# Optimization experiments

Measured on AMD Instinct MI355X. Metric: run time of the kernel, lower is better.

The kernel has to match this reference:

```python
import jax, jax.numpy as jnp
import numpy as np

NUM_LEVELS = 16
COARSEST = 16
FINEST = 1024
TABLE_SIZE = 524288  # max_hash_table_entries per level
FEAT = 2             # hash_table_feature_dim
DENSITY_W = 64
COLOR_W = 64
N_POINTS = 262144

PRIMES = jnp.array([1, 2654435761, 805459861], dtype=jnp.uint32)
# 8 cube corners: 1 -> ceil coordinate, 0 -> floor coordinate (matches source vertex_0..vertex_7)
CORNER_SEL = np.array([[1,1,1],[1,1,0],[1,0,1],[0,1,1],[1,0,0],[0,1,0],[0,0,1],[0,0,0]], dtype=bool)


def hash_encode(position, hash_table):
    # position: (N,3) in [0,1); hash_table: (NUM_LEVELS*TABLE_SIZE, FEAT)
    levels = jnp.arange(NUM_LEVELS)
    growth = jnp.exp((jnp.log(float(FINEST)) - jnp.log(float(COARSEST))) / (NUM_LEVELS - 1))
    scalings = jnp.floor(COARSEST * growth ** levels)            # (L,)
    scaled = position[:, None, :] * scalings[None, :, None]       # (N,L,3)
    floor = jnp.floor(scaled)
    ceil = jnp.ceil(scaled)
    sel = jnp.asarray(CORNER_SEL)[None, None]                     # (1,1,8,3)
    corners = jnp.where(sel, ceil[:, :, None, :], floor[:, :, None, :]).astype(jnp.uint32)  # (N,L,8,3)
    h = corners * PRIMES                                          # uint32 wrap-around mul
    idx = jnp.bitwise_xor(jnp.bitwise_xor(h[..., 0], h[..., 1]), h[..., 2]) % TABLE_SIZE
    idx = idx + (levels[None, :, None] * TABLE_SIZE).astype(jnp.uint32)  # (N,L,8)
    feats = hash_table[idx]                                       # (N,L,8,F) gather
    frac = scaled - floor                                         # (N,L,3)
    w = jnp.prod(jnp.where(sel, frac[:, :, None, :], 1.0 - frac[:, :, None, :]), axis=-1)  # (N,L,8)
    out = jnp.sum(feats * w[..., None], axis=2)                   # trilinear interp -> (N,L,F)
    return out.reshape(out.shape[0], NUM_LEVELS * FEAT)           # (N,32)


def sh_encode(d):
    # fourth-order spherical harmonics, vectorized over (N,3)
    x, y, z = d[:, 0], d[:, 1], d[:, 2]
    xx, yy, zz = x * x, y * y, z * z
    comps = [
        0.28209479177387814 * jnp.ones_like(x),
        0.4886025119029199 * y,
        0.4886025119029199 * z,
        0.4886025119029199 * x,
        1.0925484305920792 * x * y,
        1.0925484305920792 * y * z,
        0.9461746957575601 * zz - 0.31539156525252,
        1.0925484305920792 * x * z,
        0.5462742152960396 * (xx - yy),
        0.5900435899266435 * y * (3 * xx - yy),
        2.890611442640554 * x * y * z,
        0.4570457994644658 * y * (5 * zz - 1),
        0.3731763325901154 * z * (5 * zz - 3),
        0.4570457994644658 * x * (5 * zz - 1),
        1.445305721320277 * z * (xx - yy),
        0.5900435899266435 * x * (xx - 3 * yy),
    ]
    return jnp.stack(comps, axis=-1)  # (N,16)


def setup_inputs() -> dict:
    key = jax.random.key(0)
    ks = jax.random.split(key, 16)
    N = N_POINTS
    position = jax.random.uniform(ks[0], (N, 3), dtype=jnp.float32)
    direction = jax.random.normal(ks[1], (N, 3), dtype=jnp.float32)
    hash_table = jax.random.normal(ks[2], (NUM_LEVELS * TABLE_SIZE, FEAT), dtype=jnp.float32) * 1e-2
    enc_dim = NUM_LEVELS * FEAT  # 32
    def dense(k, fi, fo):
        return jax.random.normal(k, (fi, fo), dtype=jnp.float32) * (1.0 / np.sqrt(fi))
    return {
        "position": position,
        "direction": direction,
        "hash_table": hash_table,
        "w_d1": dense(ks[3], enc_dim, DENSITY_W), "b_d1": jnp.zeros((DENSITY_W,), jnp.float32),
        "w_d2": dense(ks[4], DENSITY_W, 16),      "b_d2": jnp.zeros((16,), jnp.float32),
        "w_c1": dense(ks[5], 16 + 16, COLOR_W),   "b_c1": jnp.zeros((COLOR_W,), jnp.float32),
        "w_c2": dense(ks[6], COLOR_W, COLOR_W),   "b_c2": jnp.zeros((COLOR_W,), jnp.float32),
        "w_c3": dense(ks[7], COLOR_W, 3),         "b_c3": jnp.zeros((3,), jnp.float32),
    }


def reference(position, direction, hash_table, w_d1, b_d1, w_d2, b_d2,
              w_c1, b_c1, w_c2, b_c2, w_c3, b_c3):
    enc_pos = hash_encode(position, hash_table)               # (N,32)
    h = jax.nn.relu(enc_pos @ w_d1 + b_d1)                    # (N,64)
    density = h @ w_d2 + b_d2                                 # (N,16)
    enc_dir = sh_encode(direction)                            # (N,16)
    x = jnp.concatenate([density, enc_dir], axis=-1)          # (N,32)
    x = jax.nn.relu(x @ w_c1 + b_c1)
    x = jax.nn.relu(x @ w_c2 + b_c2)
    x = x @ w_c3 + b_c3                                       # (N,3)
    color = jax.nn.sigmoid(x)                                 # high_dynamic_range=False
    return (density, color)
```

## Files before the change

### kernel.cpp

```cpp
#include <hip/hip_runtime.h>
#include <stdint.h>

#define NPTS 262144
#define TBL 524288u
#define TBL_MASK 524287u
#define NBINS 32768

#define WS_TAB_OFF   0u
#define WS_TAB_BYTES (11u * 524288u * 4u)
#define WS_ENC_OFF   WS_TAB_BYTES
#define WS_ENC_BYTES (16u * (uint32_t)NPTS * 4u)
#define WS_W_OFF     (WS_ENC_OFF + WS_ENC_BYTES)
#define WS_W_U32     4736
#define WS_HIST_OFF  (WS_W_OFF + WS_W_U32 * 4u)
#define WS_KEY_OFF   (WS_HIST_OFF + NBINS * 4u)
#define WS_IDX_OFF   (WS_KEY_OFF + (uint32_t)NPTS * 4u)
#define WS_PS_OFF    (WS_IDX_OFF + (uint32_t)NPTS * 4u)
#define WS_DS_OFF    (WS_PS_OFF + (uint32_t)NPTS * 12u)
#define WS_NEED_SORT ((size_t)WS_DS_OFF + (size_t)NPTS * 12u)
#define WS_NEED      ((size_t)WS_HIST_OFF)

#define PW_D1 0
#define PW_D2 1024
#define PW_C1 1536
#define PW_C2 2560
#define PW_C3 4608

typedef __attribute__((ext_vector_type(8))) _Float16 half8;
typedef __attribute__((ext_vector_type(4))) float f32x4;

__device__ const float d_scale[16] = {16.f, 21.f, 27.f, 36.f, 48.f, 64.f, 84.f, 111.f,
                                      147.f, 194.f, 256.f, 337.f, 445.f, 588.f, 776.f, 1024.f};

__device__ const uint16_t SEG_START[8][4] = {
    {0, 512, 683, 1024},
    {0, 512, 683, 854},
    {0, 512, 682, 1024},
    {0, 512, 768, 1024},
    {0, 512, 768, 1024},
    {0, 512, 768, 1024},
    {0, 512, 768, 1024},
    {0, 512, 1024, 1024},
};
__device__ const int8_t SEG_LEV[8][4] = {
    {9, 7, 2, 0}, {10, 7, 2, 1}, {11, 7, 1, 0}, {12, 6, 0, 0},
    {13, 6, 0, 0}, {14, 4, 3, 0}, {15, 4, 3, 0}, {8, 5, 0, 0},
};
__device__ const uint16_t SEG_CB[8][4] = {
    {0, 0, 0, 0}, {0, 171, 341, 0}, {0, 342, 170, 0}, {0, 0, 0, 0},
    {0, 256, 256, 0}, {0, 0, 0, 0}, {0, 256, 256, 0}, {0, 0, 0, 0},
};

__device__ __forceinline__ uint16_t f2h(float f) {
    _Float16 h = (_Float16)f;
    return __builtin_bit_cast(uint16_t, h);
}
__device__ __forceinline__ uint32_t pack2(float lo, float hi) {
    return (uint32_t)f2h(lo) | ((uint32_t)f2h(hi) << 16);
}
__device__ __forceinline__ float h2f_lo(uint32_t v) {
    return (float)__builtin_bit_cast(_Float16, (uint16_t)(v & 0xffffu));
}
__device__ __forceinline__ float h2f_hi(uint32_t v) {
    return (float)__builtin_bit_cast(_Float16, (uint16_t)(v >> 16));
}

__device__ __forceinline__ half8 bfrag_p(const uint32_t* __restrict__ Wp, int N, int kofs, int nofs, int l) {
    const int kp0 = (kofs + ((l >> 4) << 3)) >> 1;
    const uint32_t* p = Wp + (size_t)kp0 * N + (nofs + (l & 15));
    union { uint32_t u[4]; half8 s; } r;
    r.u[0] = p[0 * N];
    r.u[1] = p[1 * N];
    r.u[2] = p[2 * N];
    r.u[3] = p[3 * N];
    return r.s;
}
__device__ __forceinline__ half8 bfrag3_p(const uint32_t* __restrict__ Wp, int kofs, int l) {
    const int kp0 = (kofs + ((l >> 4) << 3)) >> 1;
    const int n = l & 15;
    union { uint32_t u[4]; half8 s; } r;
    if (n < 3) {
        const uint32_t* p = Wp + (size_t)kp0 * 4 + n;
        r.u[0] = p[0]; r.u[1] = p[4]; r.u[2] = p[8]; r.u[3] = p[12];
    } else {
        r.u[0] = 0; r.u[1] = 0; r.u[2] = 0; r.u[3] = 0;
    }
    return r.s;
}

__device__ __forceinline__ half8 ld_a_h(const unsigned char* hcb, int mt, int kb, int l) {
    const int row = mt * 16 + (l & 15);
    uint32_t byte = (uint32_t)row * 128 + (uint32_t)kb * 64 + (uint32_t)((l >> 4) << 4);
    byte ^= (uint32_t)(row & 7) << 4;
    return *(const half8*)(hcb + byte);
}
__device__ __forceinline__ void st_h(unsigned char* hcb, int row, int col, float v) {
    uint32_t byte = (uint32_t)row * 128 + (uint32_t)col * 2;
    byte ^= (uint32_t)(row & 7) << 4;
    *(uint16_t*)(hcb + byte) = f2h(fmaxf(v, 0.f));
}

#define MFMA(a, b, c) __builtin_amdgcn_mfma_f32_16x16x32_f16((a), (b), (c), 0, 0, 0)

__device__ __forceinline__ uint32_t spread3(uint32_t x) {
    x &= 0x3FFu;
    x = (x | (x << 16)) & 0x030000FFu;
    x = (x | (x << 8))  & 0x0300F00Fu;
    x = (x | (x << 4))  & 0x030C30C3u;
    x = (x | (x << 2))  & 0x09249249u;
    return x;
}

__global__ void __launch_bounds__(256) khist(
    const float* __restrict__ g_pos, uint32_t* __restrict__ key, uint32_t* __restrict__ hist)
{
    const int p = blockIdx.x * 256 + threadIdx.x;
    const float px = g_pos[3 * p + 0];
    const float py = g_pos[3 * p + 1];
    const float pz = g_pos[3 * p + 2];
    const uint32_t cx = min(31u, (uint32_t)(px * 32.f));
    const uint32_t cy = min(31u, (uint32_t)(py * 32.f));
    const uint32_t cz = min(31u, (uint32_t)(pz * 32.f));
    const uint32_t k = spread3(cx) | (spread3(cy) << 1) | (spread3(cz) << 2);
    key[p] = k;
    atomicAdd(&hist[k], 1u);
}

__global__ void __launch_bounds__(1024) kscan(uint32_t* __restrict__ hist) {
    const int tid = threadIdx.x;
    const int lane = tid & 63, wid = tid >> 6;
    uint4* hp = (uint4*)(hist + tid * 32);
    uint4 a[8];
    #pragma unroll
    for (int i = 0; i < 8; ++i) a[i] = hp[i];
    uint32_t S = 0;
    #pragma unroll
    for (int i = 0; i < 8; ++i) S += a[i].x + a[i].y + a[i].z + a[i].w;

    uint32_t s = S;
    #pragma unroll
    for (int d = 1; d < 64; d <<= 1) {
        const uint32_t t = __shfl_up(s, d);
        if (lane >= d) s += t;
    }
    __shared__ uint32_t ws[16];
    if (lane == 63) ws[wid] = s;
    __syncthreads();
    uint32_t woff = 0;
    for (int w = 0; w < wid; ++w) woff += ws[w];
    uint32_t run = woff + (s - S);

    #pragma unroll
    for (int i = 0; i < 8; ++i) {
        uint4 v = a[i];
        uint4 o;
        o.x = run; run += v.x;
        o.y = run; run += v.y;
        o.z = run; run += v.z;
        o.w = run; run += v.w;
        hp[i] = o;
    }
}

__global__ void __launch_bounds__(256) convert_scatter(
    const float4* __restrict__ t5,
    uint4* __restrict__ o,
    const float* __restrict__ wd1, const float* __restrict__ wd2,
    const float* __restrict__ wc1, const float* __restrict__ wc2,
    const float* __restrict__ wc3, uint32_t* __restrict__ wp,
    const float* __restrict__ g_pos, const float* __restrict__ g_dir,
    const uint32_t* __restrict__ key,
    uint32_t* __restrict__ hist, uint32_t* __restrict__ out_idx,
    float* __restrict__ pos_sorted, float* __restrict__ dir_sorted,
    const int scatter_blocks)
{
    const int blk = blockIdx.x;
    if (blk < scatter_blocks) {
        const int p = blk * 256 + threadIdx.x;
        const uint32_t slot = atomicAdd(&hist[key[p]], 1u);
        out_idx[slot] = (uint32_t)p;
        pos_sorted[3 * slot + 0] = g_pos[3 * p + 0];
        pos_sorted[3 * slot + 1] = g_pos[3 * p + 1];
        pos_sorted[3 * slot + 2] = g_pos[3 * p + 2];
        dir_sorted[3 * slot + 0] = g_dir[3 * p + 0];
        dir_sorted[3 * slot + 1] = g_dir[3 * p + 1];
        dir_sorted[3 * slot + 2] = g_dir[3 * p + 2];
    } else {
        const int cb = blk - scatter_blocks;
        const int i = cb * 256 + threadIdx.x;
        const float4 a = t5[2 * i];
        const float4 b = t5[2 * i + 1];
        o[i] = make_uint4(pack2(a.x, a.y), pack2(a.z, a.w),
                          pack2(b.x, b.y), pack2(b.z, b.w));
        if (cb == 0) {
            const int tid = threadIdx.x;
            for (int j = tid; j < 1024; j += 256) {
                const int kp = j >> 6, n = j & 63;
                wp[PW_D1 + j] = pack2(wd1[(2 * kp) * 64 + n], wd1[(2 * kp + 1) * 64 + n]);
            }
            for (int j = tid; j < 512; j += 256) {
                const int kp = j >> 4, n = j & 15;
                wp[PW_D2 + j] = pack2(wd2[(2 * kp) * 16 + n], wd2[(2 * kp + 1) * 16 + n]);
            }
            for (int j = tid; j < 1024; j += 256) {
                const int kp = j >> 6, n = j & 63;
                wp[PW_C1 + j] = pack2(wc1[(2 * kp) * 64 + n], wc1[(2 * kp + 1) * 64 + n]);
            }
            for (int j = tid; j < 2048; j += 256) {
                const int kp = j >> 6, n = j & 63;
                wp[PW_C2 + j] = pack2(wc2[(2 * kp) * 64 + n], wc2[(2 * kp + 1) * 64 + n]);
            }
            for (int j = tid; j < 128; j += 256) {
                const int kp = j >> 2, n = j & 3;
                wp[PW_C3 + j] = (n < 3) ? pack2(wc3[(2 * kp) * 3 + n], wc3[(2 * kp + 1) * 3 + n]) : 0u;
            }
        }
    }
}

__global__ void __launch_bounds__(256) gather_enc2(
    const float* __restrict__ pos,
    const float* __restrict__ g_tab32,
    const uint32_t* __restrict__ tab16,
    uint32_t* __restrict__ enc)
{
    const int b = blockIdx.x;
    const int x8 = b & 7;
    const int sslot = b >> 3;
    int seg = 0;
    #pragma unroll
    for (int i = 1; i < 4; ++i) seg = (sslot >= (int)SEG_START[x8][i]) ? i : seg;
    const int lev = SEG_LEV[x8][seg];
    const int chunk = (int)SEG_CB[x8][seg] + (sslot - (int)SEG_START[x8][seg]);
    const int pbase = (chunk << 9) + threadIdx.x;

    const float s = d_scale[lev];

    float tx[2], ty[2], tz[2];
    uint32_t idx0[2][4], idx1[2][4];
    bool odd[2];
    #pragma unroll
    for (int q = 0; q < 2; ++q) {
        const int p = pbase + q * 256;
        const float px = pos[3 * p + 0];
        const float py = pos[3 * p + 1];
        const float pz = pos[3 * p + 2];
        const float sx = px * s, sy = py * s, sz = pz * s;
        const float fx = floorf(sx), fy = floorf(sy), fz = floorf(sz);
        tx[q] = sx - fx; ty[q] = sy - fy; tz[q] = sz - fz;
        const uint32_t x0 = (uint32_t)fx, x1 = (uint32_t)ceilf(sx);
        const uint32_t hy0 = (uint32_t)fy * 2654435761u, hy1 = (uint32_t)ceilf(sy) * 2654435761u;
        const uint32_t hz0 = (uint32_t)fz * 805459861u,  hz1 = (uint32_t)ceilf(sz) * 805459861u;
        odd[q] = (x0 & 1u) != 0u;
        #pragma unroll
        for (int cp = 0; cp < 4; ++cp) {
            const uint32_t hyz = ((cp & 1) ? hy1 : hy0) ^ ((cp & 2) ? hz1 : hz0);
            idx0[q][cp] = (x0 ^ hyz) & TBL_MASK;
            idx1[q][cp] = (x1 ^ hyz) & TBL_MASK;
        }
    }

    float e[2][2] = {{0.f, 0.f}, {0.f, 0.f}};
    if (lev >= 5) {
        const uint32_t* t = tab16 + (size_t)(lev - 5) * TBL;
        uint2 v2[2][4];
        #pragma unroll
        for (int q = 0; q < 2; ++q)
            #pragma unroll
            for (int cp = 0; cp < 4; ++cp)
                v2[q][cp] = *reinterpret_cast<const uint2*>(t + (idx0[q][cp] & ~1u));
        uint32_t fup[2][4];
        #pragma unroll
        for (int q = 0; q < 2; ++q)
            #pragma unroll
            for (int cp = 0; cp < 4; ++cp)
                fup[q][cp] = odd[q] ? t[idx1[q][cp]] : 0u;
        #pragma unroll
        for (int q = 0; q < 2; ++q) {
            #pragma unroll
            for (int cp = 0; cp < 4; ++cp) {
                const bool lo = (idx0[q][cp] & 1u) == 0u;
                const uint32_t v0 = lo ? v2[q][cp].x : v2[q][cp].y;
                uint32_t v1 = lo ? v2[q][cp].y : v2[q][cp].x;
                if (odd[q]) v1 = fup[q][cp];
                const float wyz = ((cp & 1) ? ty[q] : 1.f - ty[q]) * ((cp & 2) ? tz[q] : 1.f - tz[q]);
                const float w0 = (1.f - tx[q]) * wyz;
                const float w1 = tx[q] * wyz;
                e[q][0] = fmaf(h2f_lo(v0), w0, fmaf(h2f_lo(v1), w1, e[q][0]));
                e[q][1] = fmaf(h2f_hi(v0), w0, fmaf(h2f_hi(v1), w1, e[q][1]));
            }
        }
    } else {
        const float2* t = (const float2*)g_tab32 + (size_t)lev * TBL;
        float4 v2[2][4];
        #pragma unroll
        for (int q = 0; q < 2; ++q)
            #pragma unroll
            for (int cp = 0; cp < 4; ++cp)
                v2[q][cp] = *reinterpret_cast<const float4*>(t + (idx0[q][cp] & ~1u));
        float2 fup[2][4];
        #pragma unroll
        for (int q = 0; q < 2; ++q)
            #pragma unroll
            for (int cp = 0; cp < 4; ++cp)
                fup[q][cp] = odd[q] ? t[idx1[q][cp]] : make_float2(0.f, 0.f);
        #pragma unroll
        for (int q = 0; q < 2; ++q) {
            #pragma unroll
            for (int cp = 0; cp < 4; ++cp) {
                const bool lo = (idx0[q][cp] & 1u) == 0u;
                const float v0x = lo ? v2[q][cp].x : v2[q][cp].z;
                const float v0y = lo ? v2[q][cp].y : v2[q][cp].w;
                float v1x = lo ? v2[q][cp].z : v2[q][cp].x;
                float v1y = lo ? v2[q][cp].w : v2[q][cp].y;
                if (odd[q]) { v1x = fup[q][cp].x; v1y = fup[q][cp].y; }
                const float wyz = ((cp & 1) ? ty[q] : 1.f - ty[q]) * ((cp & 2) ? tz[q] : 1.f - tz[q]);
                const float w0 = (1.f - tx[q]) * wyz;
                const float w1 = tx[q] * wyz;
                e[q][0] = fmaf(v0x, w0, fmaf(v1x, w1, e[q][0]));
                e[q][1] = fmaf(v0y, w0, fmaf(v1y, w1, e[q][1]));
            }
        }
    }
    #pragma unroll
    for (int q = 0; q < 2; ++q)
        enc[(size_t)lev * NPTS + pbase + q * 256] = pack2(e[q][0], e[q][1]);
}

__global__ void __launch_bounds__(256, 3) nerf_mlp(
    const float* __restrict__ g_dir,
    const uint32_t* __restrict__ enc,
    const uint32_t* __restrict__ wp,
    const uint32_t* __restrict__ out_idx,
    const int use_perm,
    const float* __restrict__ g_bd1,
    const float* __restrict__ g_bd2,
    const float* __restrict__ g_bc1,
    const float* __restrict__ g_bc2,
    const float* __restrict__ g_bc3,
    float* __restrict__ g_out)
{
    __shared__ __align__(16) unsigned char s_lds[4 * 12288];
    unsigned char* wbase = s_lds + (threadIdx.x >> 6) * 12288;
    unsigned char* hcb  = wbase;
    unsigned char* xinb = wbase + 8192;

    const int l = threadIdx.x & 63;
    const int m_my = l >> 4;
    const int r_my = l & 15;
    const int wpt  = blockIdx.x * 256 + (threadIdx.x & 192);
    const int p    = wpt + l;

    #pragma unroll
    for (int kb = 0; kb < 4; ++kb) {
        uint4 w4;
        w4.x = enc[(size_t)(4 * kb + 0) * NPTS + p];
        w4.y = enc[(size_t)(4 * kb + 1) * NPTS + p];
        w4.z = enc[(size_t)(4 * kb + 2) * NPTS + p];
        w4.w = enc[(size_t)(4 * kb + 3) * NPTS + p];
        *(uint4*)(hcb + m_my * 1024 + (kb * 16 + r_my) * 16) = w4;
    }

    const float dx = g_dir[3 * p + 0];
    const float dy = g_dir[3 * p + 1];
    const float dz = g_dir[3 * p + 2];

    {
        const float xx = dx * dx, yy = dy * dy, zz = dz * dz;
        float s[16];
        s[0]  = 0.28209479177387814f;
        s[1]  = 0.4886025119029199f * dy;
        s[2]  = 0.4886025119029199f * dz;
        s[3]  = 0.4886025119029199f * dx;
        s[4]  = 1.0925484305920792f * dx * dy;
        s[5]  = 1.0925484305920792f * dy * dz;
        s[6]  = 0.9461746957575601f * zz - 0.31539156525252f;
        s[7]  = 1.0925484305920792f * dx * dz;
        s[8]  = 0.5462742152960396f * (xx - yy);
        s[9]  = 0.5900435899266435f * dy * (3.f * xx - yy);
        s[10] = 2.890611442640554f * dx * dy * dz;
        s[11] = 0.4570457994644658f * dy * (5.f * zz - 1.f);
        s[12] = 0.3731763325901154f * dz * (5.f * zz - 3.f);
        s[13] = 0.4570457994644658f * dx * (5.f * zz - 1.f);
        s[14] = 1.445305721320277f * dz * (xx - yy);
        s[15] = 0.5900435899266435f * dx * (xx - 3.f * yy);
        *(uint4*)(xinb + m_my * 1024 + (32 + r_my) * 16) =
            make_uint4(pack2(s[0], s[1]), pack2(s[2], s[3]), pack2(s[4], s[5]), pack2(s[6], s[7]));
        *(uint4*)(xinb + m_my * 1024 + (48 + r_my) * 16) =
            make_uint4(pack2(s[8], s[9]), pack2(s[10], s[11]), pack2(s[12], s[13]), pack2(s[14], s[15]));
    }

    const int cl = l & 15;
    const int rg = (l >> 4) << 2;

    {
        f32x4 acc[4][4];
        half8 B[4];
        #pragma unroll
        for (int nt = 0; nt < 4; ++nt) {
            B[nt] = bfrag_p(wp + PW_D1, 64, 0, nt * 16, l);
            const float b = g_bd1[nt * 16 + cl];
            #pragma unroll
            for (int mt = 0; mt < 4; ++mt) acc[mt][nt] = (f32x4){b, b, b, b};
        }
        #pragma unroll
        for (int mt = 0; mt < 4; ++mt) {
            const half8 A = *(const half8*)(hcb + mt * 1024 + l * 16);
            #pragma unroll
            for (int nt = 0; nt < 4; ++nt) acc[mt][nt] = MFMA(A, B[nt], acc[mt][nt]);
        }
        #pragma unroll
        for (int mt = 0; mt < 4; ++mt)
            #pragma unroll
            for (int nt = 0; nt < 4; ++nt)
                #pragma unroll
                for (int r = 0; r < 4; ++r)
                    st_h(hcb, mt * 16 + rg + r, nt * 16 + cl, acc[mt][nt][r]);
    }

    {
        const half8 B0 = bfrag_p(wp + PW_D2, 16, 0,  0, l);
        const half8 B1 = bfrag_p(wp + PW_D2, 16, 32, 0, l);
        const float b = g_bd2[cl];
        #pragma unroll
        for (int mt = 0; mt < 4; ++mt) {
            f32x4 acc = (f32x4){b, b, b, b};
            acc = MFMA(ld_a_h(hcb, mt, 0, l), B0, acc);
            acc = MFMA(ld_a_h(hcb, mt, 1, l), B1, acc);
            #pragma unroll
            for (int r = 0; r < 4; ++r) {
                const int pt = wpt + mt * 16 + rg + r;
                const uint32_t opt = use_perm ? out_idx[pt] : (uint32_t)pt;
                g_out[(size_t)opt * 16 + cl] = acc[r];
                const uint32_t byte = (uint32_t)mt * 1024
                                    + (uint32_t)(((cl >> 3) * 16 + rg + r) * 16) + (uint32_t)(cl & 7) * 2;
                *(uint16_t*)(xinb + byte) = f2h(acc[r]);
            }
        }
    }

    {
        f32x4 acc[4][4];
        half8 B[4];
        #pragma unroll
        for (int nt = 0; nt < 4; ++nt) {
            B[nt] = bfrag_p(wp + PW_C1, 64, 0, nt * 16, l);
            const float b = g_bc1[nt * 16 + cl];
            #pragma unroll
            for (int mt = 0; mt < 4; ++mt) acc[mt][nt] = (f32x4){b, b, b, b};
        }
        #pragma unroll
        for (int mt = 0; mt < 4; ++mt) {
            const half8 A = *(const half8*)(xinb + mt * 1024 + l * 16);
            #pragma unroll
            for (int nt = 0; nt < 4; ++nt) acc[mt][nt] = MFMA(A, B[nt], acc[mt][nt]);
        }
        #pragma unroll
        for (int mt = 0; mt < 4; ++mt)
            #pragma unroll
            for (int nt = 0; nt < 4; ++nt)
                #pragma unroll
                for (int r = 0; r < 4; ++r)
                    st_h(hcb, mt * 16 + rg + r, nt * 16 + cl, acc[mt][nt][r]);
    }

    {
        f32x4 acc[4][4];
        #pragma unroll
        for (int nt = 0; nt < 4; ++nt) {
            const float b = g_bc2[nt * 16 + cl];
            #pragma unroll
            for (int mt = 0; mt < 4; ++mt) acc[mt][nt] = (f32x4){b, b, b, b};
        }
        #pragma unroll
        for (int kb = 0; kb < 2; ++kb) {
            half8 A[4];
            #pragma unroll
            for (int mt = 0; mt < 4; ++mt) A[mt] = ld_a_h(hcb, mt, kb, l);
            #pragma unroll
            for (int nt = 0; nt < 4; ++nt) {
                const half8 B = bfrag_p(wp + PW_C2, 64, kb * 32, nt * 16, l);
                #pragma unroll
                for (int mt = 0; mt < 4; ++mt) acc[mt][nt] = MFMA(A[mt], B, acc[mt][nt]);
            }
        }
        #pragma unroll
        for (int mt = 0; mt < 4; ++mt)
            #pragma unroll
            for (int nt = 0; nt < 4; ++nt)
                #pragma unroll
                for (int r = 0; r < 4; ++r)
                    st_h(hcb, mt * 16 + rg + r, nt * 16 + cl, acc[mt][nt][r]);
    }

    {
        const half8 B0 = bfrag3_p(wp + PW_C3, 0, l);
        const half8 B1 = bfrag3_p(wp + PW_C3, 32, l);
        const float b = (cl < 3) ? g_bc3[cl] : 0.f;
        #pragma unroll
        for (int mt = 0; mt < 4; ++mt) {
            f32x4 acc = (f32x4){b, b, b, b};
            acc = MFMA(ld_a_h(hcb, mt, 0, l), B0, acc);
            acc = MFMA(ld_a_h(hcb, mt, 1, l), B1, acc);
            if (cl < 3) {
                #pragma unroll
                for (int r = 0; r < 4; ++r) {
                    const int pt = wpt + mt * 16 + rg + r;
                    const uint32_t opt = use_perm ? out_idx[pt] : (uint32_t)pt;
                    g_out[(size_t)NPTS * 16 + (size_t)opt * 3 + cl] = 1.f / (1.f + expf(-acc[r]));
                }
            }
        }
    }
}

extern "C" void kernel_launch(void* const* d_in, const int* in_sizes, int n_in,
                              void* d_out, int out_size, void* d_ws, size_t ws_size,
                              hipStream_t stream) {
    uint32_t* tab16 = (uint32_t*)((char*)d_ws + WS_TAB_OFF);
    uint32_t* enc   = (uint32_t*)((char*)d_ws + WS_ENC_OFF);
    uint32_t* wpk   = (uint32_t*)((char*)d_ws + WS_W_OFF);
    uint32_t* hist  = (uint32_t*)((char*)d_ws + WS_HIST_OFF);
    uint32_t* key   = (uint32_t*)((char*)d_ws + WS_KEY_OFF);
    uint32_t* oidx  = (uint32_t*)((char*)d_ws + WS_IDX_OFF);
    float*    psort = (float*)((char*)d_ws + WS_PS_OFF);
    float*    dsort = (float*)((char*)d_ws + WS_DS_OFF);

    const float* g_pos = (const float*)d_in[0];
    const float* g_dir = (const float*)d_in[1];
    const float* g_tab = (const float*)d_in[2];
    const float4* t5 = (const float4*)(g_tab + (size_t)2 * 5 * TBL);

    if (ws_size >= WS_NEED_SORT) {
        hipMemsetAsync(hist, 0, NBINS * 4, stream);
        khist<<<NPTS / 256, 256, 0, stream>>>(g_pos, key, hist);
        kscan<<<1, 1024, 0, stream>>>(hist);
        convert_scatter<<<1024 + 5632, 256, 0, stream>>>(
            t5, (uint4*)tab16,
            (const float*)d_in[3], (const float*)d_in[5],
            (const float*)d_in[7], (const float*)d_in[9],
            (const float*)d_in[11], wpk,
            g_pos, g_dir, key, hist, oidx, psort, dsort, 1024);
        gather_enc2<<<8192, 256, 0, stream>>>(psort, g_tab, tab16, enc);
        nerf_mlp<<<NPTS / 256, 256, 0, stream>>>(
            dsort, enc, wpk, oidx, 1,
            (const float*)d_in[4], (const float*)d_in[6],
            (const float*)d_in[8], (const float*)d_in[10],
            (const float*)d_in[12],
            (float*)d_out);
    } else {
        convert_scatter<<<5632, 256, 0, stream>>>(
            t5, (uint4*)tab16,
            (const float*)d_in[3], (const float*)d_in[5],
            (const float*)d_in[7], (const float*)d_in[9],
            (const float*)d_in[11], wpk,
            g_pos, g_dir, nullptr, nullptr, nullptr, nullptr, nullptr, 0);
        gather_enc2<<<8192, 256, 0, stream>>>(g_pos, g_tab, tab16, enc);
        nerf_mlp<<<NPTS / 256, 256, 0, stream>>>(
            g_dir, enc, wpk, nullptr, 0,
            (const float*)d_in[4], (const float*)d_in[6],
            (const float*)d_in[8], (const float*)d_in[10],
            (const float*)d_in[12],
            (float*)d_out);
    }
}
```

Baseline: 164.2 us.

## Split gather and MLP into chunks and overlap second gather with first MLP

```diff
diff --git a/kernel.cpp b/kernel.cpp
--- a/kernel.cpp
+++ b/kernel.cpp
@@ -5,6 +5,12 @@
 #define TBL 524288u
 #define TBL_MASK 524287u
 #define NBINS 32768
+
+#define CH_A 320
+#define CH_B 192
+#define GB_BLOCKS (16 * CH_B)
+#define MA_BLOCKS (CH_A * 2)
+#define MB_BLOCKS (CH_B * 2)
 
 #define WS_TAB_OFF   0u
 #define WS_TAB_BYTES (11u * 524288u * 4u)
@@ -31,25 +37,6 @@
 
 __device__ const float d_scale[16] = {16.f, 21.f, 27.f, 36.f, 48.f, 64.f, 84.f, 111.f,
                                       147.f, 194.f, 256.f, 337.f, 445.f, 588.f, 776.f, 1024.f};
-
-__device__ const uint16_t SEG_START[8][4] = {
-    {0, 512, 683, 1024},
-    {0, 512, 683, 854},
-    {0, 512, 682, 1024},
-    {0, 512, 768, 1024},
-    {0, 512, 768, 1024},
-    {0, 512, 768, 1024},
-    {0, 512, 768, 1024},
-    {0, 512, 1024, 1024},
-};
-__device__ const int8_t SEG_LEV[8][4] = {
-    {9, 7, 2, 0}, {10, 7, 2, 1}, {11, 7, 1, 0}, {12, 6, 0, 0},
-    {13, 6, 0, 0}, {14, 4, 3, 0}, {15, 4, 3, 0}, {8, 5, 0, 0},
-};
-__device__ const uint16_t SEG_CB[8][4] = {
-    {0, 0, 0, 0}, {0, 171, 341, 0}, {0, 342, 170, 0}, {0, 0, 0, 0},
-    {0, 256, 256, 0}, {0, 0, 0, 0}, {0, 256, 256, 0}, {0, 0, 0, 0},
-};
 
 __device__ __forceinline__ uint16_t f2h(float f) {
     _Float16 h = (_Float16)f;
@@ -218,20 +205,16 @@
     }
 }
 
-__global__ void __launch_bounds__(256) gather_enc2(
+__device__ __forceinline__ void gather_body(
+    const int b, const int chunk_lo,
     const float* __restrict__ pos,
     const float* __restrict__ g_tab32,
     const uint32_t* __restrict__ tab16,
     uint32_t* __restrict__ enc)
 {
-    const int b = blockIdx.x;
     const int x8 = b & 7;
-    const int sslot = b >> 3;
-    int seg = 0;
-    #pragma unroll
-    for (int i = 1; i < 4; ++i) seg = (sslot >= (int)SEG_START[x8][i]) ? i : seg;
-    const int lev = SEG_LEV[x8][seg];
-    const int chunk = (int)SEG_CB[x8][seg] + (sslot - (int)SEG_START[x8][seg]);
+    const int lev = ((b >> 3) & 1) ? (15 - x8) : x8;
+    const int chunk = chunk_lo + (b >> 4);
     const int pbase = (chunk << 9) + threadIdx.x;
 
     const float s = d_scale[lev];
@@ -327,7 +310,18 @@
         enc[(size_t)lev * NPTS + pbase + q * 256] = pack2(e[q][0], e[q][1]);
 }
 
-__global__ void __launch_bounds__(256, 3) nerf_mlp(
+__global__ void __launch_bounds__(256) gather_range(
+    const float* __restrict__ pos,
+    const float* __restrict__ g_tab32,
+    const uint32_t* __restrict__ tab16,
+    uint32_t* __restrict__ enc,
+    const int chunk_lo)
+{
+    gather_body(blockIdx.x, chunk_lo, pos, g_tab32, tab16, enc);
+}
+
+__device__ __forceinline__ void mlp_body(
+    unsigned char* wbase, const int blk ,
     const float* __restrict__ g_dir,
     const uint32_t* __restrict__ enc,
     const uint32_t* __restrict__ wp,
@@ -340,15 +334,13 @@
     const float* __restrict__ g_bc3,
     float* __restrict__ g_out)
 {
-    __shared__ __align__(16) unsigned char s_lds[4 * 12288];
-    unsigned char* wbase = s_lds + (threadIdx.x >> 6) * 12288;
     unsigned char* hcb  = wbase;
     unsigned char* xinb = wbase + 8192;
 
     const int l = threadIdx.x & 63;
     const int m_my = l >> 4;
     const int r_my = l & 15;
-    const int wpt  = blockIdx.x * 256 + (threadIdx.x & 192);
+    const int wpt  = blk * 256 + (threadIdx.x & 192);
     const int p    = wpt + l;
 
     #pragma unroll
@@ -514,6 +506,50 @@
     }
 }
 
+__global__ void __launch_bounds__(256, 3) gatherB_mlpA(
+    const float* __restrict__ pos,
+    const float* __restrict__ g_tab32,
+    const uint32_t* __restrict__ tab16,
+    uint32_t* __restrict__ enc,
+    const float* __restrict__ dsort,
+    const uint32_t* __restrict__ wp,
+    const uint32_t* __restrict__ out_idx,
+    const float* __restrict__ g_bd1,
+    const float* __restrict__ g_bd2,
+    const float* __restrict__ g_bc1,
+    const float* __restrict__ g_bc2,
+    const float* __restrict__ g_bc3,
+    float* __restrict__ g_out)
+{
+    __shared__ __align__(16) unsigned char s_lds[4 * 12288];
+    const int b = blockIdx.x;
+    if (b < GB_BLOCKS) {
+        gather_body(b, CH_A, pos, g_tab32, tab16, enc);
+    } else {
+        mlp_body(s_lds + (threadIdx.x >> 6) * 12288, b - GB_BLOCKS,
+                 dsort, enc, wp, out_idx, 1, g_bd1, g_bd2, g_bc1, g_bc2, g_bc3, g_out);
+    }
+}
+
+__global__ void __launch_bounds__(256, 3) nerf_mlp(
+    const float* __restrict__ g_dir,
+    const uint32_t* __restrict__ enc,
+    const uint32_t* __restrict__ wp,
+    const uint32_t* __restrict__ out_idx,
+    const int use_perm,
+    const int blk_ofs,
+    const float* __restrict__ g_bd1,
+    const float* __restrict__ g_bd2,
+    const float* __restrict__ g_bc1,
+    const float* __restrict__ g_bc2,
+    const float* __restrict__ g_bc3,
+    float* __restrict__ g_out)
+{
+    __shared__ __align__(16) unsigned char s_lds[4 * 12288];
+    mlp_body(s_lds + (threadIdx.x >> 6) * 12288, blk_ofs + blockIdx.x,
+             g_dir, enc, wp, out_idx, use_perm, g_bd1, g_bd2, g_bc1, g_bc2, g_bc3, g_out);
+}
+
 extern "C" void kernel_launch(void* const* d_in, const int* in_sizes, int n_in,
                               void* d_out, int out_size, void* d_ws, size_t ws_size,
                               hipStream_t stream) {
@@ -541,9 +577,16 @@
             (const float*)d_in[7], (const float*)d_in[9],
             (const float*)d_in[11], wpk,
             g_pos, g_dir, key, hist, oidx, psort, dsort, 1024);
-        gather_enc2<<<8192, 256, 0, stream>>>(psort, g_tab, tab16, enc);
-        nerf_mlp<<<NPTS / 256, 256, 0, stream>>>(
-            dsort, enc, wpk, oidx, 1,
+        gather_range<<<16 * CH_A, 256, 0, stream>>>(psort, g_tab, tab16, enc, 0);
+        gatherB_mlpA<<<GB_BLOCKS + MA_BLOCKS, 256, 0, stream>>>(
+            psort, g_tab, tab16, enc,
+            dsort, wpk, oidx,
+            (const float*)d_in[4], (const float*)d_in[6],
+            (const float*)d_in[8], (const float*)d_in[10],
+            (const float*)d_in[12],
+            (float*)d_out);
+        nerf_mlp<<<MB_BLOCKS, 256, 0, stream>>>(
+            dsort, enc, wpk, oidx, 1, MA_BLOCKS,
             (const float*)d_in[4], (const float*)d_in[6],
             (const float*)d_in[8], (const float*)d_in[10],
             (const float*)d_in[12],
@@ -555,9 +598,9 @@
             (const float*)d_in[7], (const float*)d_in[9],
             (const float*)d_in[11], wpk,
             g_pos, g_dir, nullptr, nullptr, nullptr, nullptr, nullptr, 0);
-        gather_enc2<<<8192, 256, 0, stream>>>(g_pos, g_tab, tab16, enc);
+        gather_range<<<16 * 512, 256, 0, stream>>>(g_pos, g_tab, tab16, enc, 0);
         nerf_mlp<<<NPTS / 256, 256, 0, stream>>>(
-            g_dir, enc, wpk, nullptr, 0,
+            g_dir, enc, wpk, nullptr, 0, 0,
             (const float*)d_in[4], (const float*)d_in[6],
             (const float*)d_in[8], (const float*)d_in[10],
             (const float*)d_in[12],
```

Result: slower. 168.2 us (+2.4%).
